# Performance work log

Hardware: AMD Instinct MI355X
Metric: run time of the kernel (lower is better)

## Reference

```python
import jax, jax.numpy as jnp
import numpy as np

M = 8192          # flattened tokens (batch*seq)
IN_FEATURES = 4096
OUT_FEATURES = 4096


def setup_inputs() -> dict:
    key = jax.random.key(0)
    k1, k2, k3 = jax.random.split(key, 3)
    # int8-valued activations and weights, stored as int32 (values in [-128, 127])
    x = jax.random.randint(k1, (M, IN_FEATURES), -128, 128, dtype=jnp.int32)
    int_weight = jax.random.randint(k2, (OUT_FEATURES, IN_FEATURES), -128, 127, dtype=jnp.int32)
    bias = (jax.random.normal(k3, (OUT_FEATURES,), dtype=jnp.float32) * 0.02).astype(jnp.float16)
    return {"x": x, "int_weight": int_weight, "bias": bias}


def reference(x, int_weight, bias):
    # x.to(torch.int8); quik int8Matmul: int8 GEMM with int32 accumulation, out = x @ W^T
    x_i8 = x.astype(jnp.int8)
    w_i8 = int_weight.astype(jnp.int8)
    acc = jax.lax.dot_general(
        x_i8, w_i8,
        dimension_numbers=(((1,), (1,)), ((), ())),  # [M, K] x [N, K] -> [M, N]
        preferred_element_type=jnp.int32,
    )
    # .to(torch.float16) then bias add (fused epilogue target)
    return acc.astype(jnp.float16) + bias
```

## Files before the change

### kernel.cpp

```cpp
#include <hip/hip_runtime.h>

#define MDIM 8192
#define NDIM 4096
#define KDIM 4096
#define BM 256
#define BN 256
#define BK 128

typedef int v4i __attribute__((ext_vector_type(4)));
typedef int v16i __attribute__((ext_vector_type(16)));

__device__ __forceinline__ unsigned pack4(int x, int y, int z, int w) {
    return (unsigned)(x & 0xff) | ((unsigned)(y & 0xff) << 8) |
           ((unsigned)(z & 0xff) << 16) | ((unsigned)w << 24);
}

__global__ __launch_bounds__(256) void pack_tiled(const int* __restrict__ x,
                                                  const int* __restrict__ w,
                                                  uint4* __restrict__ xp,
                                                  uint4* __restrict__ wp) {
    __shared__ unsigned lds32[256 * 33];
    const int wg  = blockIdx.x;
    const int tid = threadIdx.x;
    const int kq   = tid & 31;
    const int rsub = tid >> 5;

    const int* src;
    uint4* dst;
    if (wg < 1024) {
        const int mtile = wg >> 5, kiter = wg & 31;
        src = x + (size_t)(mtile * 256) * KDIM + kiter * 128;
        dst = xp + (size_t)(mtile * 32 + kiter) * 2048;
    } else {
        const int ntile = (wg - 1024) >> 5, kiter = wg & 31;
        src = w + (size_t)(ntile * 256) * KDIM + kiter * 128;
        dst = wp + (size_t)(ntile * 32 + kiter) * 2048;
    }
#pragma unroll
    for (int it = 0; it < 32; ++it) {
        const int row = it * 8 + rsub;
        int4 v = *(const int4*)(src + (size_t)row * KDIM + kq * 4);
        lds32[row * 33 + kq] = pack4(v.x, v.y, v.z, v.w);
    }
    __syncthreads();
#pragma unroll
    for (int it = 0; it < 8; ++it) {
        const int g = it * 256 + tid;
        const int kb = g >> 8, row = g & 255;
        const unsigned* p = &lds32[row * 33 + kb * 4];
        uint4 o;
        o.x = p[0]; o.y = p[1]; o.z = p[2]; o.w = p[3];
        dst[g] = o;
    }
}

__global__ __launch_bounds__(512, 2) void gemm_i8_hold(const char* __restrict__ Ap,
                                                       const char* __restrict__ Bp,
                                                       const _Float16* __restrict__ bias,
                                                       _Float16* __restrict__ out) {
    __shared__ __align__(16) char lds[131072];

    const int tid  = threadIdx.x;
    const int lane = tid & 63;
    const int wave = tid >> 6;
    const int wr   = wave >> 2;
    const int wcn  = wave & 3;
    const int l31  = lane & 31;
    const int kg   = lane >> 5;

    const int lid = blockIdx.y * 16 + blockIdx.x;
    const int xc  = lid & 7, ii = lid >> 3;
    const int bx  = (xc & 3) * 4 + (ii & 3);
    const int by  = (xc >> 2) * 16 + (ii >> 2);
    const int bm0 = by * BM;
    const int bn0 = bx * BN;

    const char* apan = Ap + (size_t)by * (BM * KDIM) + tid * 16;
    const char* bpan = Bp + (size_t)bx * (BN * KDIM) + tid * 16;

    int aoff[4], boff[2];
#pragma unroll
    for (int mt = 0; mt < 4; ++mt)
        aoff[mt] = (wr * 128 + mt * 32 + l31) * 16 + kg * 4096;
#pragma unroll
    for (int nt = 0; nt < 2; ++nt)
        boff[nt] = (wcn * 64 + nt * 32 + l31) * 16 + kg * 4096;

    v16i acc[4][2];
#pragma unroll
    for (int mt = 0; mt < 4; ++mt)
#pragma unroll
        for (int nt = 0; nt < 2; ++nt)
#pragma unroll
            for (int i = 0; i < 16; ++i) acc[mt][nt][i] = 0;

    v4i afP[4], afQ[4];
    v4i bfE[2][2], bfL[2][2];

    auto stageA = [&](int nb) {
#pragma unroll
        for (int c2 = 0; c2 < 4; ++c2)
            __builtin_amdgcn_global_load_lds(
                (__attribute__((address_space(1))) const void*)(apan + c2 * 8192),
                (__attribute__((address_space(3))) void*)(lds + nb + c2 * 8192 + tid * 16),
                16, 0, 0);
    };
    auto stageB = [&](int nb) {
#pragma unroll
        for (int c2 = 0; c2 < 4; ++c2)
            __builtin_amdgcn_global_load_lds(
                (__attribute__((address_space(1))) const void*)(bpan + c2 * 8192),
                (__attribute__((address_space(3))) void*)(lds + nb + 32768 + c2 * 8192 + tid * 16),
                16, 0, 0);
    };
    auto readA = [&](v4i (&d)[4], int base, int ks) {
#pragma unroll
        for (int mt = 0; mt < 4; ++mt)
            d[mt] = *(const v4i*)(lds + base + ks * 8192 + aoff[mt]);
    };
    auto readB2 = [&](v4i (&d)[2][2], int base, int ksb) {
#pragma unroll
        for (int nt = 0; nt < 2; ++nt)
#pragma unroll
            for (int k = 0; k < 2; ++k)
                d[nt][k] = *(const v4i*)(lds + base + 32768 + (ksb + k) * 8192 + boff[nt]);
    };
    auto cl = [&](const v4i (&a)[4], const v4i (&b)[2][2], int k) {
        __builtin_amdgcn_s_setprio(1);
#pragma unroll
        for (int mt = 0; mt < 4; ++mt)
#pragma unroll
            for (int nt = 0; nt < 2; ++nt)
                acc[mt][nt] = __builtin_amdgcn_mfma_i32_32x32x32_i8(
                    a[mt], b[nt][k], acc[mt][nt], 0, 0, 0);
        __builtin_amdgcn_s_setprio(0);
    };

#define SB0 __builtin_amdgcn_sched_barrier(0)
#define TOPBAR do { asm volatile("s_waitcnt vmcnt(0)" ::: "memory"); \
                    __builtin_amdgcn_s_barrier(); } while (0)

    stageA(0); stageB(0);
    apan += BM * BK; bpan += BN * BK;
    TOPBAR; SB0;
    readB2(bfE, 0, 0);
    readA(afP, 0, 0);
    SB0;
    stageA(65536); stageB(65536);
    apan += BM * BK; bpan += BN * BK;
    SB0;
    readA(afQ, 0, 1);
    readB2(bfL, 0, 2);
    SB0;
    cl(afP, bfE, 0);
    SB0;
    readA(afP, 0, 2);
    SB0;
    cl(afQ, bfE, 1);
    SB0;
    readA(afQ, 0, 3);
    SB0;

#pragma unroll 1
    for (int t = 1; t < 32; ++t) {
        const int cur = (t & 1) ? 65536 : 0;
        TOPBAR; SB0;
        readB2(bfE, cur, 0);
        SB0;
        cl(afP, bfL, 0);
        SB0;
        readA(afP, cur, 0);
        SB0;
        cl(afQ, bfL, 1);
        SB0;
        if (t < 31) {
            stageA(cur ^ 65536);
            stageB(cur ^ 65536);
            apan += BM * BK; bpan += BN * BK;
        }
        readA(afQ, cur, 1);
        readB2(bfL, cur, 2);
        SB0;
        cl(afP, bfE, 0);
        SB0;
        readA(afP, cur, 2);
        SB0;
        cl(afQ, bfE, 1);
        SB0;
        readA(afQ, cur, 3);
        SB0;
    }
    cl(afP, bfL, 0);
    cl(afQ, bfL, 1);

#undef SB0
#undef TOPBAR

    const _Float16 bv0 = bias[bn0 + wcn * 64 + l31];
    const _Float16 bv1 = bias[bn0 + wcn * 64 + 32 + l31];
#pragma unroll
    for (int mt = 0; mt < 4; ++mt) {
#pragma unroll
        for (int nt = 0; nt < 2; ++nt) {
            const int gcol = bn0 + wcn * 64 + nt * 32 + l31;
            const _Float16 bb = nt ? bv1 : bv0;
#pragma unroll
            for (int r = 0; r < 16; ++r) {
                const int rit  = (r & 3) + 8 * (r >> 2) + 4 * kg;
                const int grow = bm0 + wr * 128 + mt * 32 + rit;
                _Float16 h = (_Float16)(float)acc[mt][nt][r] + bb;
                out[(size_t)grow * NDIM + gcol] = h;
            }
        }
    }
}

__global__ __launch_bounds__(256, 2) void gemm_i8_fb(const int* __restrict__ A32,
                                                     const int* __restrict__ B32,
                                                     const _Float16* __restrict__ bias,
                                                     _Float16* __restrict__ out) {
    __shared__ char lds[32768];
    const int tid  = threadIdx.x;
    const int lane = tid & 63;
    const int wave = tid >> 6;
    const int bm0 = blockIdx.y * 256;
    const int bn0 = blockIdx.x * 128;
    const int wr  = wave >> 1;
    const int wc  = wave & 1;
    const int l31 = lane & 31;
    const int kg  = lane >> 5;

    int abase[4];
#pragma unroll
    for (int mt = 0; mt < 4; ++mt)
        abase[mt] = kg * 4096 + (wr * 128 + mt * 32 + l31) * 16;

    v16i acc[4][2];
#pragma unroll
    for (int mt = 0; mt < 4; ++mt)
#pragma unroll
        for (int nt = 0; nt < 2; ++nt)
#pragma unroll
            for (int i = 0; i < 16; ++i) acc[mt][nt][i] = 0;

    int aoffs[8];
#pragma unroll
    for (int r = 0; r < 8; ++r) {
        const int c = r * 4 + wave;
        aoffs[r] = (bm0 + (c & 3) * 64 + lane) * KDIM + (c >> 2) * 16;
    }
    for (int k0 = 0; k0 < KDIM; k0 += 128) {
        v4i bfx[2][4];
#pragma unroll
        for (int r = 0; r < 8; ++r) {
            const int c = r * 4 + wave;
            const int4* s = (const int4*)(A32 + (size_t)aoffs[r]);
            int4 v0 = s[0], v1 = s[1], v2 = s[2], v3 = s[3];
            uint4 pk;
            pk.x = pack4(v0.x, v0.y, v0.z, v0.w);
            pk.y = pack4(v1.x, v1.y, v1.z, v1.w);
            pk.z = pack4(v2.x, v2.y, v2.z, v2.w);
            pk.w = pack4(v3.x, v3.y, v3.z, v3.w);
            *(uint4*)(lds + c * 1024 + lane * 16) = pk;
            aoffs[r] += 128;
        }
#pragma unroll
        for (int nt = 0; nt < 2; ++nt)
#pragma unroll
            for (int ks = 0; ks < 4; ++ks) {
                const int* s = B32 + (size_t)(bn0 + wc * 64 + nt * 32 + l31) * KDIM
                               + k0 + (2 * ks + kg) * 16;
                int4 v0 = ((const int4*)s)[0], v1 = ((const int4*)s)[1];
                int4 v2 = ((const int4*)s)[2], v3 = ((const int4*)s)[3];
                bfx[nt][ks][0] = (int)pack4(v0.x, v0.y, v0.z, v0.w);
                bfx[nt][ks][1] = (int)pack4(v1.x, v1.y, v1.z, v1.w);
                bfx[nt][ks][2] = (int)pack4(v2.x, v2.y, v2.z, v2.w);
                bfx[nt][ks][3] = (int)pack4(v3.x, v3.y, v3.z, v3.w);
            }
        __syncthreads();
#pragma unroll
        for (int ks = 0; ks < 4; ++ks) {
            v4i afr[4];
#pragma unroll
            for (int mt = 0; mt < 4; ++mt)
                afr[mt] = *(const v4i*)(lds + abase[mt] + ks * 8192);
#pragma unroll
            for (int mt = 0; mt < 4; ++mt)
#pragma unroll
                for (int nt = 0; nt < 2; ++nt)
                    acc[mt][nt] = __builtin_amdgcn_mfma_i32_32x32x32_i8(
                        afr[mt], bfx[nt][ks], acc[mt][nt], 0, 0, 0);
        }
        __syncthreads();
    }

    const _Float16 bv0 = bias[bn0 + wc * 64 + l31];
    const _Float16 bv1 = bias[bn0 + wc * 64 + 32 + l31];
#pragma unroll
    for (int mt = 0; mt < 4; ++mt) {
#pragma unroll
        for (int nt = 0; nt < 2; ++nt) {
            const int gcol = bn0 + wc * 64 + nt * 32 + l31;
            const _Float16 bb = nt ? bv1 : bv0;
#pragma unroll
            for (int r = 0; r < 16; ++r) {
                const int rit  = (r & 3) + 8 * (r >> 2) + 4 * kg;
                const int grow = bm0 + wr * 128 + mt * 32 + rit;
                _Float16 h = (_Float16)(float)acc[mt][nt][r] + bb;
                out[(size_t)grow * NDIM + gcol] = h;
            }
        }
    }
}

extern "C" void kernel_launch(void* const* d_in, const int* in_sizes, int n_in,
                              void* d_out, int out_size, void* d_ws, size_t ws_size,
                              hipStream_t stream) {
    const int* x = (const int*)d_in[0];
    const int* w = (const int*)d_in[1];
    const _Float16* bias = (const _Float16*)d_in[2];
    _Float16* out = (_Float16*)d_out;

    const size_t xbytes = (size_t)MDIM * KDIM;
    const size_t wbytes = (size_t)NDIM * KDIM;

    if (ws_size >= xbytes + wbytes) {
        char* xp = (char*)d_ws;
        char* wp = xp + xbytes;
        pack_tiled<<<1536, 256, 0, stream>>>(x, w, (uint4*)xp, (uint4*)wp);
        gemm_i8_hold<<<dim3(NDIM / BN, MDIM / BM), 512, 0, stream>>>(
            (const char*)xp, (const char*)wp, bias, out);
    } else {
        gemm_i8_fb<<<dim3(NDIM / 128, MDIM / 256), 256, 0, stream>>>(
            x, w, bias, out);
    }
}
```

Measured before the change: 377.5 us.

## Split waves into two phase-shifted schedules to stagger MFMA and LDS reads

Waves are split by row group into two code paths with different instruction orderings inside the K loop. One group does its MFMA clusters right after the barrier and then its LDS reads, while the other interleaves them with a one-cluster phase offset. The goal is for the two halves of the workgroup to alternate between matrix-core work and LDS traffic, so that LDS bandwidth and MFMA pipes are used at the same time instead of in lockstep. B fragment reads are also split per k-slot to better match this interleave. The cost is duplicated code, higher instruction-cache pressure, and possible register pressure from keeping more fragments live.

```diff
diff --git a/kernel.cpp b/kernel.cpp
--- a/kernel.cpp
+++ b/kernel.cpp
@@ -54,10 +54,10 @@
     }
 }
 
-__global__ __launch_bounds__(512, 2) void gemm_i8_hold(const char* __restrict__ Ap,
-                                                       const char* __restrict__ Bp,
-                                                       const _Float16* __restrict__ bias,
-                                                       _Float16* __restrict__ out) {
+__global__ __launch_bounds__(512, 2) void gemm_i8_ap(const char* __restrict__ Ap,
+                                                     const char* __restrict__ Bp,
+                                                     const _Float16* __restrict__ bias,
+                                                     _Float16* __restrict__ out) {
     __shared__ __align__(16) char lds[131072];
 
     const int tid  = threadIdx.x;
@@ -118,12 +118,10 @@
         for (int mt = 0; mt < 4; ++mt)
             d[mt] = *(const v4i*)(lds + base + ks * 8192 + aoff[mt]);
     };
-    auto readB2 = [&](v4i (&d)[2][2], int base, int ksb) {
+    auto readBk = [&](v4i (&d)[2][2], int base, int ks, int slot) {
 #pragma unroll
         for (int nt = 0; nt < 2; ++nt)
-#pragma unroll
-            for (int k = 0; k < 2; ++k)
-                d[nt][k] = *(const v4i*)(lds + base + 32768 + (ksb + k) * 8192 + boff[nt]);
+            d[nt][slot] = *(const v4i*)(lds + base + 32768 + ks * 8192 + boff[nt]);
     };
     auto cl = [&](const v4i (&a)[4], const v4i (&b)[2][2], int k) {
         __builtin_amdgcn_s_setprio(1);
@@ -143,55 +141,70 @@
     stageA(0); stageB(0);
     apan += BM * BK; bpan += BN * BK;
     TOPBAR; SB0;
-    readB2(bfE, 0, 0);
-    readA(afP, 0, 0);
-    SB0;
-    stageA(65536); stageB(65536);
-    apan += BM * BK; bpan += BN * BK;
-    SB0;
-    readA(afQ, 0, 1);
-    readB2(bfL, 0, 2);
-    SB0;
-    cl(afP, bfE, 0);
-    SB0;
-    readA(afP, 0, 2);
-    SB0;
-    cl(afQ, bfE, 1);
-    SB0;
-    readA(afQ, 0, 3);
-    SB0;
+
+    if (wr == 0) {
+        readA(afP, 0, 0); readBk(bfE, 0, 0, 0); SB0;
+        readA(afQ, 0, 1); readBk(bfE, 0, 1, 1); SB0;
+        stageA(65536); stageB(65536);
+        apan += BM * BK; bpan += BN * BK;
+        SB0;
+        cl(afP, bfE, 0); SB0;
+        readA(afP, 0, 2); readBk(bfL, 0, 2, 0); SB0;
+        cl(afQ, bfE, 1); SB0;
+        readA(afQ, 0, 3); readBk(bfL, 0, 3, 1); SB0;
 
 #pragma unroll 1
-    for (int t = 1; t < 32; ++t) {
-        const int cur = (t & 1) ? 65536 : 0;
-        TOPBAR; SB0;
-        readB2(bfE, cur, 0);
+        for (int t = 1; t < 32; ++t) {
+            const int cur = (t & 1) ? 65536 : 0;
+            TOPBAR; SB0;
+            cl(afP, bfL, 0); SB0;
+            cl(afQ, bfL, 1); SB0;
+            readA(afP, cur, 0); readBk(bfE, cur, 0, 0); SB0;
+            readA(afQ, cur, 1); readBk(bfE, cur, 1, 1); SB0;
+            if (t < 31) {
+                stageA(cur ^ 65536); stageB(cur ^ 65536);
+                apan += BM * BK; bpan += BN * BK;
+            }
+            SB0;
+            cl(afP, bfE, 0); SB0;
+            readA(afP, cur, 2); readBk(bfL, cur, 2, 0); SB0;
+            cl(afQ, bfE, 1); SB0;
+            readA(afQ, cur, 3); readBk(bfL, cur, 3, 1); SB0;
+        }
+        cl(afP, bfL, 0);
+        cl(afQ, bfL, 1);
+    } else {
+        readA(afP, 0, 0); readBk(bfE, 0, 0, 0); SB0;
+        readA(afQ, 0, 1); readBk(bfE, 0, 1, 1); SB0;
+        stageA(65536); stageB(65536);
+        apan += BM * BK; bpan += BN * BK;
         SB0;
-        cl(afP, bfL, 0);
-        SB0;
-        readA(afP, cur, 0);
-        SB0;
+        cl(afP, bfE, 0); SB0;
+        readA(afP, 0, 2); readBk(bfL, 0, 2, 0); SB0;
+        cl(afQ, bfE, 1); SB0;
+        readA(afQ, 0, 3); readBk(bfL, 0, 3, 1); SB0;
+        cl(afP, bfL, 0); SB0;
+
+#pragma unroll 1
+        for (int t = 1; t < 32; ++t) {
+            const int cur = (t & 1) ? 65536 : 0;
+            TOPBAR; SB0;
+            readA(afP, cur, 0); readBk(bfE, cur, 0, 0); SB0;
+            cl(afQ, bfL, 1); SB0;
+            readA(afQ, cur, 1); readBk(bfE, cur, 1, 1); SB0;
+            cl(afP, bfE, 0); SB0;
+            if (t < 31) {
+                stageA(cur ^ 65536); stageB(cur ^ 65536);
+                apan += BM * BK; bpan += BN * BK;
+            }
+            SB0;
+            readA(afP, cur, 2); readBk(bfL, cur, 2, 0); SB0;
+            cl(afQ, bfE, 1); SB0;
+            readA(afQ, cur, 3); readBk(bfL, cur, 3, 1); SB0;
+            cl(afP, bfL, 0); SB0;
+        }
         cl(afQ, bfL, 1);
-        SB0;
-        if (t < 31) {
-            stageA(cur ^ 65536);
-            stageB(cur ^ 65536);
-            apan += BM * BK; bpan += BN * BK;
-        }
-        readA(afQ, cur, 1);
-        readB2(bfL, cur, 2);
-        SB0;
-        cl(afP, bfE, 0);
-        SB0;
-        readA(afP, cur, 2);
-        SB0;
-        cl(afQ, bfE, 1);
-        SB0;
-        readA(afQ, cur, 3);
-        SB0;
-    }
-    cl(afP, bfL, 0);
-    cl(afQ, bfL, 1);
+    }
 
 #undef SB0
 #undef TOPBAR
@@ -328,7 +341,7 @@
         char* xp = (char*)d_ws;
         char* wp = xp + xbytes;
         pack_tiled<<<1536, 256, 0, stream>>>(x, w, (uint4*)xp, (uint4*)wp);
-        gemm_i8_hold<<<dim3(NDIM / BN, MDIM / BM), 512, 0, stream>>>(
+        gemm_i8_ap<<<dim3(NDIM / BN, MDIM / BM), 512, 0, stream>>>(
             (const char*)xp, (const char*)wp, bias, out);
     } else {
         gemm_i8_fb<<<dim3(NDIM / 128, MDIM / 256), 256, 0, stream>>>(
```

After: 377.5 us. No clear change (+0.0%).
